# Kernel optimization log

Measured on AMD Instinct MI355X. Metric: run time of the kernel, lower is better.

Reference implementation:

```python
import jax, jax.numpy as jnp
import numpy as np
import math

NEG = -10000.0  # module uses -10000, not -inf


def setup_inputs() -> dict:
    key = jax.random.key(0)
    k1, k2, k3 = jax.random.split(key, 3)
    B, Sq, Sk, H, Hkv, D = 2, 2048, 2048, 16, 4, 64
    q = jax.random.normal(k1, (B, Sq, H, D), dtype=jnp.float32)
    kv = jax.random.normal(k2, (B, Sk, 2, Hkv, D), dtype=jnp.float32)
    key_padding_mask = jax.random.randint(k3, (B, Sk), 0, 2) > 0  # True = valid key
    return {"q": q, "kv": kv, "key_padding_mask": key_padding_mask}


def reference(q, kv, key_padding_mask):
    B, Sq, H, D = q.shape
    Sk, Hkv = kv.shape[1], kv.shape[3]
    if Hkv != H:
        # einops repeat '... hkv d -> ... (hkv g) d': each kv head repeated g times contiguously
        kv = jnp.repeat(kv, H // Hkv, axis=3)
    k, v = kv[:, :, 0], kv[:, :, 1]  # [B, Sk, H, D] each
    scale = 1.0 / math.sqrt(D)
    scores = jnp.einsum('bthd,bshd->bhts', q, k * scale)  # [B, H, Sq, Sk]
    # key padding: additive 0 where valid, -10000 where padded
    pad = jnp.where(key_padding_mask, 0.0, NEG).astype(scores.dtype)
    scores = scores + pad[:, None, None, :]
    # causal mask: cols > rows + Sk - Sq gets replaced (not added) with -10000
    rows = jnp.arange(Sq)[:, None]
    cols = jnp.arange(Sk)[None, :]
    causal_mask = cols > rows + (Sk - Sq)
    scores = jnp.where(causal_mask, NEG, scores)
    attention = jax.nn.softmax(scores, axis=-1).astype(v.dtype)
    # dropout p=0.0 -> identity
    output = jnp.einsum('bhts,bshd->bthd', attention, v)  # [B, Sq, H, D]
    return output
```

## Files before the change

### kernel.cpp

```cpp
#include <hip/hip_runtime.h>
#include <math.h>


typedef __bf16 bf16x4 __attribute__((ext_vector_type(4)));
typedef __bf16 bf16x8 __attribute__((ext_vector_type(8)));
typedef float floatx4 __attribute__((ext_vector_type(4)));
typedef short shortx4 __attribute__((ext_vector_type(4)));

#define SQ 2048
#define SK 2048
#define H_ 16
#define HKV 4
#define D_ 64
#define QT 64
#define KT 64
#define KVROW 512
#define NEGV (-10000.0f)
#define QSCL 0.18033688f
#define EBIAS 17.3123405f

static __device__ __forceinline__ floatx4 mfma16(bf16x4 a, bf16x4 b, floatx4 c) {
#if __has_builtin(__builtin_amdgcn_mfma_f32_16x16x16bf16_1k)
    return __builtin_amdgcn_mfma_f32_16x16x16bf16_1k(
        __builtin_bit_cast(shortx4, a), __builtin_bit_cast(shortx4, b), c, 0, 0, 0);
#else
    floatx4 d;
    asm("v_mfma_f32_16x16x16_bf16 %0, %1, %2, %3"
        : "=v"(d) : "v"(a), "v"(b), "v"(c));
    return d;
#endif
}

static __device__ __forceinline__ void gload16(const void* g, void* l) {
    __builtin_amdgcn_global_load_lds(
        (const __attribute__((address_space(1))) unsigned int*)g,
        (__attribute__((address_space(3))) unsigned int*)l, 16, 0, 0);
}

__global__ __launch_bounds__(256)
void prep_kernel(const float* __restrict__ kv, const int* __restrict__ mask,
                 char* __restrict__ imgs)
{
    __shared__ alignas(16) __bf16 Vl[64][64];
    const int tid = threadIdx.x;
    const int bid = (int)blockIdx.x;
    const int kt = bid & 31, hkv = (bid >> 5) & 3, b = bid >> 7;
    const float* kvb = kv + ((size_t)b * SK + kt * KT) * KVROW + hkv * D_;
    const float* vvb = kvb + HKV * D_;
    char* img = imgs + ((size_t)bid << 15);

    const int r  = tid >> 2;
    const int gg = tid & 3;

    {
        const float* p = kvb + (size_t)r * KVROW + gg * 16;
        float4 f0 = *(const float4*)(p + 0), f1 = *(const float4*)(p + 4);
        float4 f2 = *(const float4*)(p + 8), f3 = *(const float4*)(p + 12);
        bf16x8 c0 = { (__bf16)f0.x, (__bf16)f0.y, (__bf16)f0.z, (__bf16)f0.w,
                      (__bf16)f1.x, (__bf16)f1.y, (__bf16)f1.z, (__bf16)f1.w };
        bf16x8 c1 = { (__bf16)f2.x, (__bf16)f2.y, (__bf16)f2.z, (__bf16)f2.w,
                      (__bf16)f3.x, (__bf16)f3.y, (__bf16)f3.z, (__bf16)f3.w };
        const int xo = (r & 7) << 4;
        *(bf16x8*)(img + r * 128 + (((gg * 2 + 0) * 16) ^ xo)) = c0;
        *(bf16x8*)(img + r * 128 + (((gg * 2 + 1) * 16) ^ xo)) = c1;
    }
    {
        const float mker = mask[b * SK + kt * KT + r] ? 1.0f : 0.0f;
        const float* p = vvb + (size_t)r * KVROW + gg * 16;
        float4 f0 = *(const float4*)(p + 0), f1 = *(const float4*)(p + 4);
        float4 f2 = *(const float4*)(p + 8), f3 = *(const float4*)(p + 12);
        float t[16] = { f0.x, f0.y, f0.z, f0.w, f1.x, f1.y, f1.z, f1.w,
                        f2.x, f2.y, f2.z, f2.w, f3.x, f3.y, f3.z, f3.w };
#pragma unroll
        for (int j = 0; j < 16; ++j)
            Vl[gg * 16 + j][r] = (__bf16)(t[j] * mker);
    }
    __syncthreads();
#pragma unroll
    for (int i = 0; i < 2; ++i) {
        const int c = tid * 2 + i, rr = c >> 3, g = c & 7;
        bf16x8 v = *(const bf16x8*)&Vl[rr][g * 8];
        *(bf16x8*)(img + 8192 + rr * 128 + ((g * 16) ^ ((rr & 7) << 4))) = v;
    }
    if (tid < 64) {
        const int m = mask[b * SK + kt * KT + tid];
        *((__bf16*)(img + 16384) + tid) = (__bf16)(m ? 1.0f : 0.0f);
    }
}

__global__ __launch_bounds__(256, 4)
void attn_kernel(const float* __restrict__ q,
                 const float* __restrict__ kv,
                 const int* __restrict__ mask,
                 float* __restrict__ out,
                 float* __restrict__ ws)
{
    __shared__ alignas(16) union {
        struct {
            __bf16 K[2][KT * D_];
            __bf16 V[2][D_ * KT];
        } m;
        struct {
            float fpart[4][64];
            float fw[4][64];
            int   s_first;
        } f;
    } sh;

    const int tid  = threadIdx.x;
    const int wave = tid >> 6;
    const int lane = tid & 63;
    const int col  = lane & 15;
    const int quad = lane >> 4;

    if (blockIdx.x < 32) {
        const int bh = (int)blockIdx.x;
        const int b = bh >> 4, h = bh & 15, hkv = h >> 2;
        if (tid == 0) sh.f.s_first = SK;
        __syncthreads();
        int local = SK;
        for (int s = tid; s < SK; s += 256)
            if (mask[b * SK + s]) local = min(local, s);
        atomicMin(&sh.f.s_first, local);
        __syncthreads();
        const int nfirst = sh.f.s_first;
        if (nfirst == 0) return;

        const float* kvb = kv + (size_t)b * SK * KVROW + hkv * D_;
        const float* vvb = kvb + HKV * D_;
        {
            float a0=0,a1=0,a2=0,a3=0,a4=0,a5=0,a6=0,a7=0;
            const int s0 = wave * 512;
            for (int s = s0; s < s0 + 512; s += 8) {
                a0 += vvb[(size_t)(s+0)*KVROW + lane];
                a1 += vvb[(size_t)(s+1)*KVROW + lane];
                a2 += vvb[(size_t)(s+2)*KVROW + lane];
                a3 += vvb[(size_t)(s+3)*KVROW + lane];
                a4 += vvb[(size_t)(s+4)*KVROW + lane];
                a5 += vvb[(size_t)(s+5)*KVROW + lane];
                a6 += vvb[(size_t)(s+6)*KVROW + lane];
                a7 += vvb[(size_t)(s+7)*KVROW + lane];
            }
            sh.f.fpart[wave][lane] = ((a0+a1)+(a2+a3)) + ((a4+a5)+(a6+a7));
        }
        __syncthreads();
        const float vtotal = sh.f.fpart[0][lane] + sh.f.fpart[1][lane]
                           + sh.f.fpart[2][lane] + sh.f.fpart[3][lane];

        for (int R = wave; R < nfirst; R += 4) {
            const float* qrow = q + (((size_t)b * SQ + R) * H_ + h) * D_;
            float mymax = -3.4e38f;
            for (int s = lane; s <= R; s += 64) {
                const float* kp = kvb + (size_t)s * KVROW;
                float dt = 0.f;
                for (int d = 0; d < D_; ++d) dt += qrow[d] * kp[d];
                mymax = fmaxf(mymax, dt * 0.125f + NEGV);
            }
#pragma unroll
            for (int off = 32; off >= 1; off >>= 1)
                mymax = fmaxf(mymax, __shfl_xor(mymax, off, 64));
            const float M = (R < SK - 1) ? fmaxf(mymax, NEGV) : mymax;
            float lsum = 0.f, oacc = 0.f, pref = 0.f;
            for (int s0 = 0; s0 <= R; s0 += 64) {
                int s = s0 + lane;
                float w = 0.f;
                if (s <= R) {
                    const float* kp = kvb + (size_t)s * KVROW;
                    float dt = 0.f;
                    for (int d = 0; d < D_; ++d) dt += qrow[d] * kp[d];
                    w = __expf(dt * 0.125f + NEGV - M);
                    lsum += w;
                }
                sh.f.fw[wave][lane] = w;
                const int nk = (R - s0 + 1 < 64) ? (R - s0 + 1) : 64;
                for (int j = 0; j < nk; ++j) {
                    const float vj = vvb[(size_t)(s0 + j) * KVROW + lane];
                    oacc += sh.f.fw[wave][j] * vj;
                    pref += vj;
                }
            }
#pragma unroll
            for (int off = 32; off >= 1; off >>= 1)
                lsum += __shfl_xor(lsum, off, 64);
            const float wn   = __expf(NEGV - M);
            const float ltot = lsum + wn * (float)(SK - 1 - R);
            out[(((size_t)b * SQ + R) * H_ + h) * D_ + lane] =
                (oacc + wn * (vtotal - pref)) / ltot;
        }
        return;
    }

    const int id = (int)blockIdx.x - 32;
    const int bh = id & 31;
    const int y  = id >> 5;
    const int kg = y >> 3, jj = y & 7;
    const int qt = (kg == 0) ? 31 - jj : (kg == 1) ? jj : (kg == 2) ? 23 - jj : 8 + jj;
    const int b = bh >> 4, h = bh & 15, hkv = h >> 2;
    const int qw = qt * QT + wave * 16;

    const char* timg0 = (const char*)ws + ((size_t)((b * 4 + hkv) * 32) << 15);

    bf16x8 aq[2];
    {
        const int row = qw + col;
        const float* qp = q + (((size_t)b * SQ + row) * H_ + h) * D_ + quad * 8;
#pragma unroll
        for (int kc = 0; kc < 2; ++kc) {
            const float* p = qp + kc * 32;
#pragma unroll
            for (int j = 0; j < 8; ++j) aq[kc][j] = (__bf16)(p[j] * QSCL);
        }
    }

    floatx4 o[4];
    floatx4 l_acc = (floatx4){0.f, 0.f, 0.f, 0.f};
#pragma unroll
    for (int dj = 0; dj < 4; ++dj) o[dj] = (floatx4){0.f, 0.f, 0.f, 0.f};

    const int c7 = col & 7;
    const int xo = c7 << 4;

    auto gstage = [&](int kt, const int bb) {
        const char* img = timg0 + ((size_t)kt << 15);
        const char* gsK = img + wave * 1024 + lane * 16;
        const char* gsV = img + 8192 + wave * 1024 + lane * 16;
        char* ldK = (char*)&sh.m.K[bb][0] + wave * 1024;
        char* ldV = (char*)&sh.m.V[bb][0] + wave * 1024;
        gload16(gsK,        ldK);
        gload16(gsK + 4096, ldK + 4096);
        gload16(gsV,        ldV);
        gload16(gsV + 4096, ldV + 4096);
    };

    auto loadmk = [&](int kt, bf16x4* mk) {
        const char* mrow = timg0 + ((size_t)kt << 15) + 16384;
#pragma unroll
        for (int kj = 0; kj < 4; ++kj)
            mk[kj] = *(const bf16x4*)(mrow + kj * 32 + quad * 8);
    };

    auto tile_body = [&](const int CUR, const int kt, const bf16x4* mk) {
        const char* Kb = (const char*)&sh.m.K[CUR][0];
        floatx4 c[4];
        __builtin_amdgcn_s_setprio(1);
#pragma unroll
        for (int kj = 0; kj < 4; ++kj) {
            c[kj] = (floatx4){-EBIAS, -EBIAS, -EBIAS, -EBIAS};
#pragma unroll
            for (int kc = 0; kc < 2; ++kc) {
                bf16x8 ak = *(const bf16x8*)(Kb + (kj * 16 + col) * 128
                                                + ((((kc * 4 + quad) ^ c7) << 4)));
                c[kj] = __builtin_amdgcn_mfma_f32_16x16x32_bf16(ak, aq[kc], c[kj], 0, 0, 0);
            }
        }
        __builtin_amdgcn_s_setprio(0);

        bf16x4 pk[4];
        if (kt == qt) {
            const int tcl = wave * 16 + col - quad * 4;
#pragma unroll
            for (int kj = 0; kj < 4; ++kj)
#pragma unroll
                for (int r = 0; r < 4; ++r) {
                    float p = __builtin_amdgcn_exp2f(c[kj][r]);
                    pk[kj][r] = (__bf16)((kj * 16 + r <= tcl) ? p : 0.f);
                }
        } else {
#pragma unroll
            for (int kj = 0; kj < 4; ++kj)
#pragma unroll
                for (int r = 0; r < 4; ++r)
                    pk[kj][r] = (__bf16)__builtin_amdgcn_exp2f(c[kj][r]);
        }

        const char* Vb = (const char*)&sh.m.V[CUR][0];
        __builtin_amdgcn_s_setprio(1);
#pragma unroll
        for (int kj = 0; kj < 4; ++kj)
            l_acc = mfma16(pk[kj], mk[kj], l_acc);
#pragma unroll
        for (int dj = 0; dj < 4; ++dj)
#pragma unroll
            for (int kj = 0; kj < 4; ++kj) {
                bf16x4 bv = *(const bf16x4*)(Vb + (dj * 16 + col) * 128
                                                + ((kj * 32 + quad * 8) ^ xo));
                o[dj] = mfma16(pk[kj], bv, o[dj]);
            }
        __builtin_amdgcn_s_setprio(0);
    };

    const int k1 = qt + 1;
    gstage(0, 0);
    int kt = 0;
    for (;;) {
        __syncthreads();
        bf16x4 mkA[4];
        loadmk(kt, mkA);
        if (kt + 1 < k1) gstage(kt + 1, 1);
        tile_body(0, kt, mkA);
        if (++kt == k1) break;
        __syncthreads();
        bf16x4 mkB[4];
        loadmk(kt, mkB);
        if (kt + 1 < k1) gstage(kt + 1, 0);
        tile_body(1, kt, mkB);
        if (++kt == k1) break;
    }

#pragma unroll
    for (int r = 0; r < 4; ++r) {
        const float l = l_acc[r];
        if (l > 0.f) {
            const float inv = 1.0f / l;
            const int row = qw + quad * 4 + r;
            float* op = out + (((size_t)b * SQ + row) * H_ + h) * D_ + col;
#pragma unroll
            for (int dj = 0; dj < 4; ++dj)
                op[dj * 16] = o[dj][r] * inv;
        }
    }
}

extern "C" void kernel_launch(void* const* d_in, const int* in_sizes, int n_in,
                              void* d_out, int out_size, void* d_ws, size_t ws_size,
                              hipStream_t stream) {
    const float* q   = (const float*)d_in[0];
    const float* kv  = (const float*)d_in[1];
    const int* mask  = (const int*)d_in[2];
    float* out       = (float*)d_out;
    prep_kernel<<<dim3(256), 256, 0, stream>>>(kv, mask, (char*)d_ws);
    attn_kernel<<<dim3(32 + 1024), 256, 0, stream>>>(q, kv, mask, out, (float*)d_ws);
}
```

Baseline: 107.8 us.

## Split long causal query tiles across KV chunks with a separate combine kernel

Causal query tiles are now split into KV chunks of eight tiles each (one to four splits depending on tile index), raising the block count from 1024 to 2560 and evening out per-block work. Split blocks write unnormalized partial outputs and row sums to workspace, and a new combine kernel sums the partials and normalizes. Launch bounds occupancy is also raised from 4 to 5. The split adds a third launch plus extra global traffic for the partials. Summing partials without per-split max rescaling relies on the fixed exponent bias already used for the softmax.

After: 121.4 us. 1.13x slower.

```diff
diff --git a/kernel.cpp b/kernel.cpp
--- a/kernel.cpp
+++ b/kernel.cpp
@@ -18,6 +18,10 @@
 #define NEGV (-10000.0f)
 #define QSCL 0.18033688f
 #define EBIAS 17.3123405f
+#define IMG_BYTES (256u << 15)
+#define PART_OFF (IMG_BYTES / 4)
+#define SLOTF 4160
+#define SLOTS_PER_BH 72
 
 static __device__ __forceinline__ floatx4 mfma16(bf16x4 a, bf16x4 b, floatx4 c) {
 #if __has_builtin(__builtin_amdgcn_mfma_f32_16x16x16bf16_1k)
@@ -88,7 +92,7 @@
     }
 }
 
-__global__ __launch_bounds__(256, 4)
+__global__ __launch_bounds__(256, 5)
 void attn_kernel(const float* __restrict__ q,
                  const float* __restrict__ kv,
                  const int* __restrict__ mask,
@@ -192,9 +196,16 @@
 
     const int id = (int)blockIdx.x - 32;
     const int bh = id & 31;
-    const int y  = id >> 5;
-    const int kg = y >> 3, jj = y & 7;
-    const int qt = (kg == 0) ? 31 - jj : (kg == 1) ? jj : (kg == 2) ? 23 - jj : 8 + jj;
+    const int z  = 79 - (id >> 5);
+    int qt, sp;
+    if (z < 8)       { qt = z;                sp = 0; }
+    else if (z < 24) { qt = 8 + ((z - 8) >> 1);  sp = (z - 8) & 1; }
+    else if (z < 48) { qt = 16 + (z - 24) / 3;   sp = (z - 24) % 3; }
+    else             { qt = 24 + ((z - 48) >> 2); sp = (z - 48) & 3; }
+    const int nsplit = 1 + (qt >> 3);
+    const int k0 = sp * 8;
+    const int k1 = min(qt + 1, k0 + 8);
+
     const int b = bh >> 4, h = bh & 15, hkv = h >> 2;
     const int qw = qt * QT + wave * 16;
 
@@ -289,9 +300,8 @@
         __builtin_amdgcn_s_setprio(0);
     };
 
-    const int k1 = qt + 1;
-    gstage(0, 0);
-    int kt = 0;
+    gstage(k0, 0);
+    int kt = k0;
     for (;;) {
         __syncthreads();
         bf16x4 mkA[4];
@@ -307,16 +317,73 @@
         if (++kt == k1) break;
     }
 
-#pragma unroll
-    for (int r = 0; r < 4; ++r) {
-        const float l = l_acc[r];
-        if (l > 0.f) {
-            const float inv = 1.0f / l;
-            const int row = qw + quad * 4 + r;
-            float* op = out + (((size_t)b * SQ + row) * H_ + h) * D_ + col;
+    if (nsplit == 1) {
+#pragma unroll
+        for (int r = 0; r < 4; ++r) {
+            const float l = l_acc[r];
+            if (l > 0.f) {
+                const float inv = 1.0f / l;
+                const int row = qw + quad * 4 + r;
+                float* op = out + (((size_t)b * SQ + row) * H_ + h) * D_ + col;
+#pragma unroll
+                for (int dj = 0; dj < 4; ++dj)
+                    op[dj * 16] = o[dj][r] * inv;
+            }
+        }
+    } else {
+        const int local0 = (qt < 16) ? (qt - 8) * 2
+                         : (qt < 24) ? 16 + (qt - 16) * 3
+                                     : 40 + (qt - 24) * 4;
+        float* slot = ws + PART_OFF
+                    + ((size_t)bh * SLOTS_PER_BH + local0 + sp) * SLOTF;
+#pragma unroll
+        for (int r = 0; r < 4; ++r) {
+            const int row = wave * 16 + quad * 4 + r;
+            float* op = slot + (size_t)row * 64 + col;
 #pragma unroll
             for (int dj = 0; dj < 4; ++dj)
-                op[dj * 16] = o[dj][r] * inv;
+                op[dj * 16] = o[dj][r];
+            if (col == 0) slot[4096 + row] = l_acc[r];
+        }
+    }
+}
+
+__global__ __launch_bounds__(256)
+void combine_kernel(const float* __restrict__ ws, float* __restrict__ out)
+{
+    __shared__ float linv[64];
+    const int tid = threadIdx.x;
+    const int bh = (int)blockIdx.x & 31;
+    const int qt = 8 + ((int)blockIdx.x >> 5);
+    const int b = bh >> 4, h = bh & 15;
+    const int n = 1 + (qt >> 3);
+    const int local0 = (qt < 16) ? (qt - 8) * 2
+                     : (qt < 24) ? 16 + (qt - 16) * 3
+                                 : 40 + (qt - 24) * 4;
+    const float* s0 = ws + PART_OFF
+                    + ((size_t)bh * SLOTS_PER_BH + local0) * SLOTF;
+
+    if (tid < 64) {
+        float s = 0.f;
+        for (int k = 0; k < n; ++k)
+            s += s0[(size_t)k * SLOTF + 4096 + tid];
+        linv[tid] = (s > 0.f) ? 1.0f / s : 0.f;
+    }
+    __syncthreads();
+
+#pragma unroll
+    for (int c = 0; c < 4; ++c) {
+        const int idx = c * 1024 + tid * 4;
+        const int row = idx >> 6, d = idx & 63;
+        float4 acc = *(const float4*)(s0 + idx);
+        for (int k = 1; k < n; ++k) {
+            const float4 t = *(const float4*)(s0 + (size_t)k * SLOTF + idx);
+            acc.x += t.x; acc.y += t.y; acc.z += t.z; acc.w += t.w;
+        }
+        const float inv = linv[row];
+        if (inv > 0.f) {
+            float4 r4 = { acc.x * inv, acc.y * inv, acc.z * inv, acc.w * inv };
+            *(float4*)(out + (((size_t)b * SQ + qt * 64 + row) * H_ + h) * D_ + d) = r4;
         }
     }
 }
@@ -329,5 +396,6 @@
     const int* mask  = (const int*)d_in[2];
     float* out       = (float*)d_out;
     prep_kernel<<<dim3(256), 256, 0, stream>>>(kv, mask, (char*)d_ws);
-    attn_kernel<<<dim3(32 + 1024), 256, 0, stream>>>(q, kv, mask, out, (float*)d_ws);
-}
+    attn_kernel<<<dim3(32 + 2560), 256, 0, stream>>>(q, kv, mask, out, (float*)d_ws);
+    combine_kernel<<<dim3(768), 256, 0, stream>>>((const float*)d_ws, out);
+}
```
